# Optimization experiments

Measured on AMD Instinct MI355X. Metric: run time of the kernel, lower is better.

The kernel has to match this reference:

```python
import jax, jax.numpy as jnp
import numpy as np

D, H, E = 1024, 4096, 8


def setup_inputs() -> dict:
    key = jax.random.key(0)
    ks = jax.random.split(key, 8)
    s_in = 1.0 / np.sqrt(D)
    s_hid = 1.0 / np.sqrt(H)
    return {
        "x": jax.random.normal(ks[0], (4, 2048, D), dtype=jnp.float32),
        # torch nn.Linear init ~ U(-1/sqrt(fan_in), 1/sqrt(fan_in)); exact dist irrelevant for a numeric reference
        "Wg": jax.random.uniform(ks[1], (D, E), jnp.float32, -s_in, s_in),
        "bg": jax.random.uniform(ks[2], (E,), jnp.float32, -s_in, s_in),
        "W1": jax.random.uniform(ks[3], (E, D, H), jnp.float32, -s_in, s_in),
        "b1": jax.random.uniform(ks[4], (E, H), jnp.float32, -s_in, s_in),
        "W2": jax.random.uniform(ks[5], (E, H, D), jnp.float32, -s_hid, s_hid),
        "b2": jax.random.uniform(ks[6], (E, D), jnp.float32, -s_hid, s_hid),
    }


def reference(x, Wg, bg, W1, b1, W2, b2):
    # gate
    gate_logits = jnp.einsum("bsd,de->bse", x, Wg) + bg
    gate_probs = jax.nn.softmax(gate_logits, axis=-1)
    expert_indices = jnp.argmax(gate_probs, axis=-1)  # [B,S]

    # Faithful to source: mask the INPUT per expert, run the full MLP on the
    # masked input (biases still apply to zeroed tokens!), and sum all experts.
    onehot = jax.nn.one_hot(expert_indices, E, dtype=x.dtype)  # [B,S,E]
    xm = jnp.einsum("bsd,bse->ebsd", x, onehot)                # [E,B,S,D]
    h = jax.nn.relu(jnp.einsum("ebsd,edh->ebsh", xm, W1) + b1[:, None, None, :])
    out_e = jnp.einsum("ebsh,ehd->ebsd", h, W2) + b2[:, None, None, :]
    combined_output = jnp.sum(out_e, axis=0)                   # [B,S,D]
    return combined_output, gate_probs, expert_indices
```

## Files before the change

### kernel.cpp

```cpp
#include <hip/hip_runtime.h>
#include <hip/hip_bf16.h>
#include <cstdint>

#define D_DIM 1024
#define H_DIM 4096
#define E_NUM 8
#define NTOK  8192

#define BM 128
#define BN 128
#define BK 64

#define MAXT 72
#define NBY1 (H_DIM / BN)
#define NBY2 (D_DIM / BN)

typedef __bf16 bf16;
typedef __bf16 bf16x8 __attribute__((ext_vector_type(8)));
typedef __bf16 bf16x4 __attribute__((ext_vector_type(4)));
typedef float  f32x4  __attribute__((ext_vector_type(4)));

#define GLOAD16(g, l)                                                          \
    __builtin_amdgcn_global_load_lds(                                          \
        (const __attribute__((address_space(1))) void*)(g),                    \
        (__attribute__((address_space(3))) void*)(l), 16, 0, 0)

#define SBAR()   asm volatile("s_barrier" ::: "memory")
#define VMCNT0() asm volatile("s_waitcnt vmcnt(0)" ::: "memory")

#define STAGE_A(bf, tt) do {                                                   \
    GLOAD16(Asrc + (size_t)(tt) * BK,               &sA[(bf)][(w * 8) * BK]);  \
    GLOAD16(Asrc + 32 * K + (size_t)(tt) * BK,      &sA[(bf)][(w * 8 + 32) * BK]); \
    GLOAD16(Asrc + 64 * K + (size_t)(tt) * BK,      &sA[(bf)][(w * 8 + 64) * BK]); \
    GLOAD16(Asrc + 96 * K + (size_t)(tt) * BK,      &sA[(bf)][(w * 8 + 96) * BK]); \
} while (0)
#define STAGE_B(bf, tt) do {                                                   \
    GLOAD16(Bsrc + (size_t)(tt) * BK,               &sB[(bf)][(w * 8) * BK]);  \
    GLOAD16(Bsrc + 32 * K + (size_t)(tt) * BK,      &sB[(bf)][(w * 8 + 32) * BK]); \
    GLOAD16(Bsrc + 64 * K + (size_t)(tt) * BK,      &sB[(bf)][(w * 8 + 64) * BK]); \
    GLOAD16(Bsrc + 96 * K + (size_t)(tt) * BK,      &sB[(bf)][(w * 8 + 96) * BK]); \
} while (0)

#define LDA(i, kh) (*(const bf16x8*)&sA[buf][((i) * 16 + wr * 64 + l15) * BK + ((kh) ? kidx1 : kidx0)])
#define LDB(j, kh) (*(const bf16x8*)&sB[buf][((j) * 16 + wc * 64 + l15) * BK + ((kh) ? kidx1 : kidx0)])

#define MMROW(I, AA) do {                                                      \
    acc[I][0] = __builtin_amdgcn_mfma_f32_16x16x32_bf16(AA, vb0, acc[I][0], 0, 0, 0); \
    acc[I][1] = __builtin_amdgcn_mfma_f32_16x16x32_bf16(AA, vb1, acc[I][1], 0, 0, 0); \
    acc[I][2] = __builtin_amdgcn_mfma_f32_16x16x32_bf16(AA, vb2, acc[I][2], 0, 0, 0); \
    acc[I][3] = __builtin_amdgcn_mfma_f32_16x16x32_bf16(AA, vb3, acc[I][3], 0, 0, 0); \
} while (0)

#define KLOOP(NT) do {                                                         \
    STAGE_A(0, 0); STAGE_B(0, 0);                                              \
    VMCNT0(); SBAR();                                                          \
    for (int kt = 0; kt < (NT); kt++) {                                        \
        const int buf = kt & 1, ob = buf ^ 1;                                  \
        const int tp1 = (kt + 1 < (NT)) ? kt + 1 : 0;                          \
        bf16x8 a0, a1, a2, a3, vb0, vb1, vb2, vb3;                             \
                                                            \
        a0 = LDA(0, 0); a1 = LDA(1, 0); a2 = LDA(2, 0); a3 = LDA(3, 0);        \
        vb0 = LDB(0, 0); vb1 = LDB(1, 0); vb2 = LDB(2, 0); vb3 = LDB(3, 0);    \
        STAGE_B(ob, tp1);                                                      \
        SBAR();                                                                \
        __builtin_amdgcn_s_setprio(1);                                         \
        MMROW(0, a0); MMROW(1, a1); MMROW(2, a2); MMROW(3, a3);                \
        __builtin_amdgcn_s_setprio(0);                                         \
        SBAR();                                                                \
                                                            \
        a0 = LDA(0, 1); a1 = LDA(1, 1); a2 = LDA(2, 1); a3 = LDA(3, 1);        \
        vb0 = LDB(0, 1); vb1 = LDB(1, 1); vb2 = LDB(2, 1); vb3 = LDB(3, 1);    \
        STAGE_A(ob, tp1);                                                      \
        SBAR();                                                                \
        __builtin_amdgcn_s_setprio(1);                                         \
        MMROW(0, a0); MMROW(1, a1); MMROW(2, a2); MMROW(3, a3);                \
        __builtin_amdgcn_s_setprio(0);                                         \
        VMCNT0();                                                              \
        SBAR();                                                                \
    }                                                                          \
} while (0)

__global__ __launch_bounds__(64) void gate_kernel(
    const float* __restrict__ x, const float* __restrict__ Wg,
    const float* __restrict__ bg, float* __restrict__ out_probs,
    float* __restrict__ out_idx, int* __restrict__ cnt, int* __restrict__ list)
{
    const int t = blockIdx.x;
    const int l = threadIdx.x;
    double part[E_NUM];
#pragma unroll
    for (int e = 0; e < E_NUM; e++) part[e] = 0.0;
    const float* xr = x + (size_t)t * D_DIM;
#pragma unroll
    for (int i = 0; i < D_DIM / 64; i++) {
        const int d = l + i * 64;
        const float xv = xr[d];
        const float* wr = Wg + (size_t)d * E_NUM;
        float4 w0 = *(const float4*)(wr);
        float4 w1 = *(const float4*)(wr + 4);
        part[0] += (double)xv * (double)w0.x;
        part[1] += (double)xv * (double)w0.y;
        part[2] += (double)xv * (double)w0.z;
        part[3] += (double)xv * (double)w0.w;
        part[4] += (double)xv * (double)w1.x;
        part[5] += (double)xv * (double)w1.y;
        part[6] += (double)xv * (double)w1.z;
        part[7] += (double)xv * (double)w1.w;
    }
#pragma unroll
    for (int e = 0; e < E_NUM; e++) {
        double v = part[e];
        for (int s = 32; s > 0; s >>= 1) v += __shfl_xor(v, s, 64);
        part[e] = v;
    }
    if (l == 0) {
        float logits[E_NUM], probs[E_NUM];
        float m = -3.0e38f;
#pragma unroll
        for (int e = 0; e < E_NUM; e++) {
            logits[e] = (float)(part[e] + (double)bg[e]);
            m = fmaxf(m, logits[e]);
        }
        float s = 0.f;
#pragma unroll
        for (int e = 0; e < E_NUM; e++) { probs[e] = expf(logits[e] - m); s += probs[e]; }
        const float inv = 1.f / s;
        int best = 0; float bp = -1.f;
#pragma unroll
        for (int e = 0; e < E_NUM; e++) {
            probs[e] *= inv;
            if (probs[e] > bp) { bp = probs[e]; best = e; }
        }
#pragma unroll
        for (int e = 0; e < E_NUM; e++) out_probs[(size_t)t * E_NUM + e] = probs[e];
        out_idx[t] = (float)best;
        const int pos = atomicAdd(&cnt[best], 1);
        list[best * NTOK + pos] = t;
    }
}

__global__ __launch_bounds__(256) void zero_kernel(int* cnt, float* cpartial)
{
    const int i = blockIdx.x * 256 + threadIdx.x;
    if (i < E_NUM * D_DIM) cpartial[i] = 0.f;
    if (i < E_NUM) cnt[i] = 0;
}

__global__ void offsets_kernel(const int* __restrict__ cnt, int* __restrict__ off,
                               int* __restrict__ tile_e, int* __restrict__ tile_row,
                               int* __restrict__ tile_n)
{
    if (threadIdx.x == 0) {
        int a = 0, n = 0;
        for (int e = 0; e < E_NUM; e++) {
            off[e] = a; a += cnt[e];
            for (int rr = 0; rr < cnt[e]; rr += BM) {
                tile_e[n] = e; tile_row[n] = rr; n++;
            }
        }
        tile_n[0] = n;
    }
}

__global__ __launch_bounds__(256) void gather_kernel(
    const float* __restrict__ x, const int* __restrict__ off,
    const int* __restrict__ cnt, const int* __restrict__ list,
    bf16* __restrict__ Xg)
{
    const int p = blockIdx.x;
    int e = 0;
    while (e < E_NUM - 1 && p >= off[e] + cnt[e]) e++;
    const int token = list[e * NTOK + (p - off[e])];
    const float* src = x + (size_t)token * D_DIM;
    bf16* dst = Xg + (size_t)p * D_DIM;
    const int t = threadIdx.x;
    float4 v = *(const float4*)(src + t * 4);
    bf16x4 o;
    o[0] = (bf16)v.x; o[1] = (bf16)v.y; o[2] = (bf16)v.z; o[3] = (bf16)v.w;
    *(bf16x4*)(dst + t * 4) = o;
}

__global__ __launch_bounds__(256) void transpose_conv_kernel(
    const float* __restrict__ in, bf16* __restrict__ out, int K, int N)
{
    const int e = blockIdx.z;
    const float* src = in + (size_t)e * K * N;
    bf16* dst = out + (size_t)e * K * N;
    __shared__ float T[64][65];
    const int t = threadIdx.x;
    const int k0 = blockIdx.x * 64, n0 = blockIdx.y * 64;
    {
        const int ty = t >> 4;
        const int tx = (t & 15) * 4;
#pragma unroll
        for (int i = 0; i < 4; i++) {
            float4 v = *(const float4*)(src + (size_t)(k0 + ty + 16 * i) * N + n0 + tx);
            T[ty + 16 * i][tx + 0] = v.x; T[ty + 16 * i][tx + 1] = v.y;
            T[ty + 16 * i][tx + 2] = v.z; T[ty + 16 * i][tx + 3] = v.w;
        }
    }
    __syncthreads();
    {
        const int n  = t >> 2;
        const int kx = (t & 3) * 16;
        bf16 tmp[16];
#pragma unroll
        for (int j = 0; j < 16; j++) tmp[j] = (bf16)T[kx + j][n];
        *(bf16x8*)(dst + (size_t)(n0 + n) * K + k0 + kx)     = *(bf16x8*)&tmp[0];
        *(bf16x8*)(dst + (size_t)(n0 + n) * K + k0 + kx + 8) = *(bf16x8*)&tmp[8];
    }
}

__global__ __launch_bounds__(256) void transpose_conv_w2_kernel(
    const float* __restrict__ in, const float* __restrict__ b1,
    bf16* __restrict__ out, float* __restrict__ cpartial)
{
    const int K = H_DIM, N = D_DIM;
    const int e = blockIdx.z;
    const float* src = in + (size_t)e * K * N;
    bf16* dst = out + (size_t)e * K * N;
    __shared__ float T[64][65];
    const int t = threadIdx.x;
    const int k0 = blockIdx.x * 64, n0 = blockIdx.y * 64;
    {
        const int ty = t >> 4;
        const int tx = (t & 15) * 4;
#pragma unroll
        for (int i = 0; i < 4; i++) {
            float4 v = *(const float4*)(src + (size_t)(k0 + ty + 16 * i) * N + n0 + tx);
            T[ty + 16 * i][tx + 0] = v.x; T[ty + 16 * i][tx + 1] = v.y;
            T[ty + 16 * i][tx + 2] = v.z; T[ty + 16 * i][tx + 3] = v.w;
        }
    }
    __syncthreads();
    {
        const int n  = t >> 2;
        const int kx = (t & 3) * 16;
        bf16 tmp[16];
#pragma unroll
        for (int j = 0; j < 16; j++) tmp[j] = (bf16)T[kx + j][n];
        *(bf16x8*)(dst + (size_t)(n0 + n) * K + k0 + kx)     = *(bf16x8*)&tmp[0];
        *(bf16x8*)(dst + (size_t)(n0 + n) * K + k0 + kx + 8) = *(bf16x8*)&tmp[8];
    }
    if (t < 64) {
        float s = 0.f;
#pragma unroll 8
        for (int h = 0; h < 64; h++)
            s += fmaxf(b1[(size_t)e * H_DIM + k0 + h], 0.f) * T[h][t];
        atomicAdd(&cpartial[(size_t)e * D_DIM + n0 + t], s);
    }
}

__global__ __launch_bounds__(256) void cfinal_kernel(
    const float* __restrict__ cpartial, const float* __restrict__ b2,
    float* __restrict__ adj)
{
    const int d = blockIdx.x * 256 + threadIdx.x;
    float c[E_NUM];
    float tot = 0.f;
#pragma unroll
    for (int e = 0; e < E_NUM; e++) {
        c[e] = cpartial[(size_t)e * D_DIM + d] + b2[(size_t)e * D_DIM + d];
        tot += c[e];
    }
#pragma unroll
    for (int e = 0; e < E_NUM; e++) adj[(size_t)e * D_DIM + d] = tot - c[e];
}

__global__ __launch_bounds__(256, 2) void gemm1_kernel(
    const bf16* __restrict__ Xg, const bf16* __restrict__ W1t,
    const float* __restrict__ b1, const int* __restrict__ cnt,
    const int* __restrict__ off, const int* __restrict__ tile_e,
    const int* __restrict__ tile_row, const int* __restrict__ tile_n,
    bf16* __restrict__ Hb)
{
    const int orig = blockIdx.x;
    const int qch = (MAXT * NBY1) >> 3;
    const int fid = (orig & 7) * qch + (orig >> 3);
    const int tx = fid / NBY1;
    const int by = fid % NBY1;
    if (tx >= tile_n[0]) return;
    const int e  = tile_e[tx];
    const int m0 = tile_row[tx];
    const int ne = cnt[e];
    const int oe = off[e];
    const int K = D_DIM;

    __shared__ bf16 sA[2][BM * BK];
    __shared__ bf16 sB[2][BN * BK];

    const int t = threadIdx.x;
    const int w = t >> 6, lane = t & 63;
    const int wr = w >> 1, wc = w & 1;
    const int l15 = lane & 15;
    const int kidx0 = (((lane >> 4)) ^ (lane & 7)) << 3;
    const int kidx1 = ((4 + (lane >> 4)) ^ (lane & 7)) << 3;

    const int srow = w * 8 + (lane >> 3);
    const int schk = (((lane & 7) ^ (lane >> 3)) << 3);
    const bf16* Asrc = Xg + (size_t)(oe + m0 + srow) * K + schk;
    const bf16* Bsrc = W1t + ((size_t)e * H_DIM + by * BN + srow) * K + schk;

    f32x4 acc[4][4];
#pragma unroll
    for (int i = 0; i < 4; i++)
#pragma unroll
        for (int j = 0; j < 4; j++) acc[i][j] = (f32x4){0.f, 0.f, 0.f, 0.f};

    KLOOP(K / BK);

    float bias[4];
#pragma unroll
    for (int j = 0; j < 4; j++)
        bias[j] = b1[(size_t)e * H_DIM + by * BN + wc * 64 + j * 16 + l15];
#pragma unroll
    for (int i = 0; i < 4; i++) {
        const int rb0 = m0 + wr * 64 + i * 16 + ((lane >> 4) << 2);
#pragma unroll
        for (int j = 0; j < 4; j++) {
            const int gcol = by * BN + wc * 64 + j * 16 + l15;
#pragma unroll
            for (int r = 0; r < 4; r++) {
                const int grow = rb0 + r;
                if (grow < ne) {
                    float v = acc[i][j][r] + bias[j];
                    Hb[((size_t)(oe + grow)) * H_DIM + gcol] = (bf16)fmaxf(v, 0.f);
                }
            }
        }
    }
}

__global__ __launch_bounds__(256, 2) void gemm2_kernel(
    const bf16* __restrict__ Hb, const bf16* __restrict__ W2t,
    const float* __restrict__ b2, const float* __restrict__ adj,
    const int* __restrict__ cnt, const int* __restrict__ off,
    const int* __restrict__ tile_e, const int* __restrict__ tile_row,
    const int* __restrict__ tile_n, const int* __restrict__ list,
    float* __restrict__ out)
{
    const int orig = blockIdx.x;
    const int qch = (MAXT * NBY2) >> 3;
    const int fid = (orig & 7) * qch + (orig >> 3);
    const int tx = fid / NBY2;
    const int by = fid % NBY2;
    if (tx >= tile_n[0]) return;
    const int e  = tile_e[tx];
    const int m0 = tile_row[tx];
    const int ne = cnt[e];
    const int oe = off[e];
    const int K = H_DIM;

    __shared__ bf16 sA[2][BM * BK];
    __shared__ bf16 sB[2][BN * BK];

    const int t = threadIdx.x;
    const int w = t >> 6, lane = t & 63;
    const int wr = w >> 1, wc = w & 1;
    const int l15 = lane & 15;
    const int kidx0 = (((lane >> 4)) ^ (lane & 7)) << 3;
    const int kidx1 = ((4 + (lane >> 4)) ^ (lane & 7)) << 3;

    const int srow = w * 8 + (lane >> 3);
    const int schk = (((lane & 7) ^ (lane >> 3)) << 3);
    const bf16* Asrc = Hb + (size_t)(oe + m0 + srow) * K + schk;
    const bf16* Bsrc = W2t + ((size_t)e * D_DIM + by * BN + srow) * K + schk;

    f32x4 acc[4][4];
#pragma unroll
    for (int i = 0; i < 4; i++)
#pragma unroll
        for (int j = 0; j < 4; j++) acc[i][j] = (f32x4){0.f, 0.f, 0.f, 0.f};

    KLOOP(K / BK);

    float badj[4];
#pragma unroll
    for (int j = 0; j < 4; j++) {
        const int gcol = by * BN + wc * 64 + j * 16 + l15;
        badj[j] = b2[(size_t)e * D_DIM + gcol] + adj[(size_t)e * D_DIM + gcol];
    }
#pragma unroll
    for (int i = 0; i < 4; i++) {
        const int rb0 = m0 + wr * 64 + i * 16 + ((lane >> 4) << 2);
#pragma unroll
        for (int j = 0; j < 4; j++) {
            const int gcol = by * BN + wc * 64 + j * 16 + l15;
#pragma unroll
            for (int r = 0; r < 4; r++) {
                const int grow = rb0 + r;
                if (grow < ne) {
                    const int tok = list[e * NTOK + grow];
                    out[(size_t)tok * D_DIM + gcol] = acc[i][j][r] + badj[j];
                }
            }
        }
    }
}

extern "C" void kernel_launch(void* const* d_in, const int* in_sizes, int n_in,
                              void* d_out, int out_size, void* d_ws, size_t ws_size,
                              hipStream_t stream)
{
    (void)in_sizes; (void)n_in; (void)out_size; (void)ws_size;
    const float* x  = (const float*)d_in[0];
    const float* Wg = (const float*)d_in[1];
    const float* bg = (const float*)d_in[2];
    const float* W1 = (const float*)d_in[3];
    const float* b1 = (const float*)d_in[4];
    const float* W2 = (const float*)d_in[5];
    const float* b2 = (const float*)d_in[6];

    float* out_comb  = (float*)d_out;
    float* out_probs = out_comb + (size_t)NTOK * D_DIM;
    float* out_idx   = out_probs + (size_t)NTOK * E_NUM;

    char* ws = (char*)d_ws;
    size_t o = 0;
    bf16* W1t = (bf16*)(ws + o); o += (size_t)E_NUM * H_DIM * D_DIM * 2;
    bf16* W2t = (bf16*)(ws + o); o += (size_t)E_NUM * H_DIM * D_DIM * 2;
    bf16* Hb  = (bf16*)(ws + o); o += (size_t)NTOK * H_DIM * 2;
    bf16* Xg  = (bf16*)(ws + o); o += (size_t)NTOK * D_DIM * 2;
    float* cpartial = (float*)(ws + o); o += (size_t)E_NUM * D_DIM * 4;
    float* adj      = (float*)(ws + o); o += (size_t)E_NUM * D_DIM * 4;
    int* cnt  = (int*)(ws + o); o += 256;
    int* off  = (int*)(ws + o); o += 256;
    int* tile_e   = (int*)(ws + o); o += 512;
    int* tile_row = (int*)(ws + o); o += 512;
    int* tile_n   = (int*)(ws + o); o += 256;
    int* list = (int*)(ws + o); o += (size_t)E_NUM * NTOK * 4;

    zero_kernel<<<(E_NUM * D_DIM + 255) / 256, 256, 0, stream>>>(cnt, cpartial);
    gate_kernel<<<NTOK, 64, 0, stream>>>(x, Wg, bg, out_probs, out_idx, cnt, list);
    offsets_kernel<<<1, 64, 0, stream>>>(cnt, off, tile_e, tile_row, tile_n);
    gather_kernel<<<NTOK, 256, 0, stream>>>(x, off, cnt, list, Xg);
    transpose_conv_kernel<<<dim3(D_DIM / 64, H_DIM / 64, E_NUM), 256, 0, stream>>>(W1, W1t, D_DIM, H_DIM);
    transpose_conv_w2_kernel<<<dim3(H_DIM / 64, D_DIM / 64, E_NUM), 256, 0, stream>>>(W2, b1, W2t, cpartial);
    cfinal_kernel<<<D_DIM / 256, 256, 0, stream>>>(cpartial, b2, adj);
    gemm1_kernel<<<MAXT * NBY1, 256, 0, stream>>>(Xg, W1t, b1, cnt, off, tile_e, tile_row, tile_n, Hb);
    gemm2_kernel<<<MAXT * NBY2, 256, 0, stream>>>(Hb, W2t, b2, adj, cnt, off, tile_e, tile_row, tile_n, list, out_comb);
}
```

Measured before the change: 512.8 us.

## Switch GEMM k-loop to 4-stage LDS ring with BK=32 and partial vmcnt waits

Replaces the double-buffered BK=64 k-loop with a four-slot LDS ring of BK=32 tiles, issuing loads three stages ahead and waiting with vmcnt(12) instead of draining all loads. Each iteration now has one barrier pair and one MFMA batch. The swizzle and row mapping are reworked to fit 32-wide rows. The aim is to hide global-load latency behind compute. In exchange the loop runs twice as many iterations and barriers, and LDS use per block stays at 64KB.

```diff
diff --git a/kernel.cpp b/kernel.cpp
--- a/kernel.cpp
+++ b/kernel.cpp
@@ -9,7 +9,7 @@
 
 #define BM 128
 #define BN 128
-#define BK 64
+#define BK 32
 
 #define MAXT 72
 #define NBY1 (H_DIM / BN)
@@ -25,24 +25,20 @@
         (const __attribute__((address_space(1))) void*)(g),                    \
         (__attribute__((address_space(3))) void*)(l), 16, 0, 0)
 
-#define SBAR()   asm volatile("s_barrier" ::: "memory")
-#define VMCNT0() asm volatile("s_waitcnt vmcnt(0)" ::: "memory")
-
-#define STAGE_A(bf, tt) do {                                                   \
-    GLOAD16(Asrc + (size_t)(tt) * BK,               &sA[(bf)][(w * 8) * BK]);  \
-    GLOAD16(Asrc + 32 * K + (size_t)(tt) * BK,      &sA[(bf)][(w * 8 + 32) * BK]); \
-    GLOAD16(Asrc + 64 * K + (size_t)(tt) * BK,      &sA[(bf)][(w * 8 + 64) * BK]); \
-    GLOAD16(Asrc + 96 * K + (size_t)(tt) * BK,      &sA[(bf)][(w * 8 + 96) * BK]); \
+#define SBAR()    asm volatile("s_barrier" ::: "memory")
+#define VMCNT12() asm volatile("s_waitcnt vmcnt(12)" ::: "memory")
+
+#define STAGE_A(sl, tt) do {                                                   \
+    GLOAD16(Asrc + (size_t)(tt) * BK,          &sA[(sl)][(w * 16) * BK]);      \
+    GLOAD16(Asrc + 64 * K + (size_t)(tt) * BK, &sA[(sl)][(64 + w * 16) * BK]); \
 } while (0)
-#define STAGE_B(bf, tt) do {                                                   \
-    GLOAD16(Bsrc + (size_t)(tt) * BK,               &sB[(bf)][(w * 8) * BK]);  \
-    GLOAD16(Bsrc + 32 * K + (size_t)(tt) * BK,      &sB[(bf)][(w * 8 + 32) * BK]); \
-    GLOAD16(Bsrc + 64 * K + (size_t)(tt) * BK,      &sB[(bf)][(w * 8 + 64) * BK]); \
-    GLOAD16(Bsrc + 96 * K + (size_t)(tt) * BK,      &sB[(bf)][(w * 8 + 96) * BK]); \
+#define STAGE_B(sl, tt) do {                                                   \
+    GLOAD16(Bsrc + (size_t)(tt) * BK,          &sB[(sl)][(w * 16) * BK]);      \
+    GLOAD16(Bsrc + 64 * K + (size_t)(tt) * BK, &sB[(sl)][(64 + w * 16) * BK]); \
 } while (0)
 
-#define LDA(i, kh) (*(const bf16x8*)&sA[buf][((i) * 16 + wr * 64 + l15) * BK + ((kh) ? kidx1 : kidx0)])
-#define LDB(j, kh) (*(const bf16x8*)&sB[buf][((j) * 16 + wc * 64 + l15) * BK + ((kh) ? kidx1 : kidx0)])
+#define LDA(i) (*(const bf16x8*)&sA[sl][((i) * 16 + wr * 64 + l15) * BK + kidx])
+#define LDB(j) (*(const bf16x8*)&sB[sl][((j) * 16 + wc * 64 + l15) * BK + kidx])
 
 #define MMROW(I, AA) do {                                                      \
     acc[I][0] = __builtin_amdgcn_mfma_f32_16x16x32_bf16(AA, vb0, acc[I][0], 0, 0, 0); \
@@ -53,29 +49,21 @@
 
 #define KLOOP(NT) do {                                                         \
     STAGE_A(0, 0); STAGE_B(0, 0);                                              \
-    VMCNT0(); SBAR();                                                          \
+    STAGE_A(1, 1); STAGE_B(1, 1);                                              \
+    STAGE_A(2, 2); STAGE_B(2, 2);                                              \
     for (int kt = 0; kt < (NT); kt++) {                                        \
-        const int buf = kt & 1, ob = buf ^ 1;                                  \
-        const int tp1 = (kt + 1 < (NT)) ? kt + 1 : 0;                          \
+        const int sl = kt & 3;                                                 \
+        const int ps = (kt + 3) & 3;                                           \
+        const int tt3 = (kt + 3 < (NT)) ? kt + 3 : kt + 3 - (NT);              \
+        STAGE_A(ps, tt3); STAGE_B(ps, tt3);                                    \
+        VMCNT12();                                                             \
+        SBAR();                                                                \
         bf16x8 a0, a1, a2, a3, vb0, vb1, vb2, vb3;                             \
-                                                            \
-        a0 = LDA(0, 0); a1 = LDA(1, 0); a2 = LDA(2, 0); a3 = LDA(3, 0);        \
-        vb0 = LDB(0, 0); vb1 = LDB(1, 0); vb2 = LDB(2, 0); vb3 = LDB(3, 0);    \
-        STAGE_B(ob, tp1);                                                      \
-        SBAR();                                                                \
+        a0 = LDA(0); a1 = LDA(1); a2 = LDA(2); a3 = LDA(3);                    \
+        vb0 = LDB(0); vb1 = LDB(1); vb2 = LDB(2); vb3 = LDB(3);                \
         __builtin_amdgcn_s_setprio(1);                                         \
         MMROW(0, a0); MMROW(1, a1); MMROW(2, a2); MMROW(3, a3);                \
         __builtin_amdgcn_s_setprio(0);                                         \
-        SBAR();                                                                \
-                                                            \
-        a0 = LDA(0, 1); a1 = LDA(1, 1); a2 = LDA(2, 1); a3 = LDA(3, 1);        \
-        vb0 = LDB(0, 1); vb1 = LDB(1, 1); vb2 = LDB(2, 1); vb3 = LDB(3, 1);    \
-        STAGE_A(ob, tp1);                                                      \
-        SBAR();                                                                \
-        __builtin_amdgcn_s_setprio(1);                                         \
-        MMROW(0, a0); MMROW(1, a1); MMROW(2, a2); MMROW(3, a3);                \
-        __builtin_amdgcn_s_setprio(0);                                         \
-        VMCNT0();                                                              \
         SBAR();                                                                \
     }                                                                          \
 } while (0)
@@ -286,18 +274,17 @@
     const int oe = off[e];
     const int K = D_DIM;
 
-    __shared__ bf16 sA[2][BM * BK];
-    __shared__ bf16 sB[2][BN * BK];
+    __shared__ bf16 sA[4][BM * BK];
+    __shared__ bf16 sB[4][BN * BK];
 
     const int t = threadIdx.x;
     const int w = t >> 6, lane = t & 63;
     const int wr = w >> 1, wc = w & 1;
     const int l15 = lane & 15;
-    const int kidx0 = (((lane >> 4)) ^ (lane & 7)) << 3;
-    const int kidx1 = ((4 + (lane >> 4)) ^ (lane & 7)) << 3;
-
-    const int srow = w * 8 + (lane >> 3);
-    const int schk = (((lane & 7) ^ (lane >> 3)) << 3);
+    const int kidx = (((lane >> 4) ^ (lane & 3)) << 3);
+
+    const int srow = w * 16 + (lane >> 2);
+    const int schk = (((lane & 3) ^ ((lane >> 2) & 3)) << 3);
     const bf16* Asrc = Xg + (size_t)(oe + m0 + srow) * K + schk;
     const bf16* Bsrc = W1t + ((size_t)e * H_DIM + by * BN + srow) * K + schk;
 
@@ -351,18 +338,17 @@
     const int oe = off[e];
     const int K = H_DIM;
 
-    __shared__ bf16 sA[2][BM * BK];
-    __shared__ bf16 sB[2][BN * BK];
+    __shared__ bf16 sA[4][BM * BK];
+    __shared__ bf16 sB[4][BN * BK];
 
     const int t = threadIdx.x;
     const int w = t >> 6, lane = t & 63;
     const int wr = w >> 1, wc = w & 1;
     const int l15 = lane & 15;
-    const int kidx0 = (((lane >> 4)) ^ (lane & 7)) << 3;
-    const int kidx1 = ((4 + (lane >> 4)) ^ (lane & 7)) << 3;
-
-    const int srow = w * 8 + (lane >> 3);
-    const int schk = (((lane & 7) ^ (lane >> 3)) << 3);
+    const int kidx = (((lane >> 4) ^ (lane & 3)) << 3);
+
+    const int srow = w * 16 + (lane >> 2);
+    const int schk = (((lane & 3) ^ ((lane >> 2) & 3)) << 3);
     const bf16* Asrc = Hb + (size_t)(oe + m0 + srow) * K + schk;
     const bf16* Bsrc = W2t + ((size_t)e * D_DIM + by * BN + srow) * K + schk;
 
```

After: 549.7 us. +7.2%, slower.
